# Performance work log

Hardware: AMD Instinct MI355X
Metric: run time of the kernel (lower is better)

Reference implementation:

```python
import jax, jax.numpy as jnp
import numpy as np

N_EMBD = 1024
N_HEAD = 16

def _lin_params(key, fan_in, fan_out):
    kw, kb = jax.random.split(key)
    bound = 1.0 / np.sqrt(fan_in)
    W = jax.random.uniform(kw, (fan_in, fan_out), minval=-bound, maxval=bound, dtype=jnp.float32)
    b = jax.random.uniform(kb, (fan_out,), minval=-bound, maxval=bound, dtype=jnp.float32)
    return W, b

def setup_inputs() -> dict:
    key = jax.random.key(0)
    ks = jax.random.split(key, 6)
    x = jax.random.normal(ks[0], (2, 2048, N_EMBD), dtype=jnp.float32)
    W_attn, b_attn = _lin_params(ks[1], N_EMBD, 3 * N_EMBD)
    W_proj, b_proj = _lin_params(ks[2], N_EMBD, N_EMBD)
    W_fc, b_fc = _lin_params(ks[3], N_EMBD, 4 * N_EMBD)
    W_fc2, b_fc2 = _lin_params(ks[4], 4 * N_EMBD, N_EMBD)
    ln1_g = jnp.ones((N_EMBD,), jnp.float32); ln1_b = jnp.zeros((N_EMBD,), jnp.float32)
    ln2_g = jnp.ones((N_EMBD,), jnp.float32); ln2_b = jnp.zeros((N_EMBD,), jnp.float32)
    return {"x": x, "W_attn": W_attn, "b_attn": b_attn, "W_proj": W_proj, "b_proj": b_proj,
            "W_fc": W_fc, "b_fc": b_fc, "W_fc2": W_fc2, "b_fc2": b_fc2,
            "ln1_g": ln1_g, "ln1_b": ln1_b, "ln2_g": ln2_g, "ln2_b": ln2_b}

def _layernorm(x, g, b, eps=1e-5):
    mu = jnp.mean(x, axis=-1, keepdims=True)
    var = jnp.var(x, axis=-1, keepdims=True)
    return (x - mu) * jax.lax.rsqrt(var + eps) * g + b

def _attention(x, W_attn, b_attn, W_proj, b_proj):
    B, T, C = x.shape
    hd = C // N_HEAD
    qkv = x @ W_attn + b_attn                      # [B,T,3C]
    q, k, v = jnp.split(qkv, 3, axis=-1)
    # [B,T,C] -> [B,H,T,hd]
    q = q.reshape(B, T, N_HEAD, hd).transpose(0, 2, 1, 3)
    k = k.reshape(B, T, N_HEAD, hd).transpose(0, 2, 1, 3)
    v = v.reshape(B, T, N_HEAD, hd).transpose(0, 2, 1, 3)
    att = jnp.einsum('bhqd,bhkd->bhqk', q, k) * (1.0 / np.sqrt(hd))
    causal = jnp.tril(jnp.ones((T, T), bool))
    att = jnp.where(causal[None, None], att, -jnp.inf)
    att = jax.nn.softmax(att, axis=-1)
    y = jnp.einsum('bhqk,bhkd->bhqd', att, v)      # [B,H,T,hd]
    y = y.transpose(0, 2, 1, 3).reshape(B, T, C)
    return y @ W_proj + b_proj

def _mlp(x, W_fc, b_fc, W_fc2, b_fc2):
    h = jax.nn.gelu(x @ W_fc + b_fc, approximate=False)
    return h @ W_fc2 + b_fc2

def reference(x, W_attn, b_attn, W_proj, b_proj, W_fc, b_fc, W_fc2, b_fc2,
              ln1_g, ln1_b, ln2_g, ln2_b):
    x = x + _attention(_layernorm(x, ln1_g, ln1_b), W_attn, b_attn, W_proj, b_proj)
    x = x + _mlp(_layernorm(x, ln2_g, ln2_b), W_fc, b_fc, W_fc2, b_fc2)
    return x
```

## Files before the change

### kernel.cpp

```cpp
#include <hip/hip_runtime.h>
#include <cstdint>
#include <cstddef>


typedef unsigned short u16;
typedef short bf16x8 __attribute__((ext_vector_type(8)));
typedef float f32x4 __attribute__((ext_vector_type(4)));

#define C_EMBD 1024
#define T_SEQ  2048
#define N_BATCH 2
#define N_HEADS 16
#define HEAD_D 64
#define M_TOK  4096
#define Q_SCALE 0.18033688011112042f

__device__ __forceinline__ u16 f2b(float f) {
  union { float f; unsigned u; } v; v.f = f;
  unsigned r = (v.u + 0x7fffu + ((v.u >> 16) & 1u)) >> 16;
  return (u16)r;
}
__device__ __forceinline__ float b2f(u16 u) {
  union { unsigned u; float f; } v; v.u = ((unsigned)u) << 16;
  return v.f;
}
__device__ __forceinline__ unsigned pk2(float a, float b) {
  union { float f; unsigned u; } x, y; x.f = a; y.f = b;
  return __builtin_amdgcn_perm(y.u, x.u, 0x07060302u);
}
__device__ __forceinline__ void load_lds16(const void* g, void* l) {
  __builtin_amdgcn_global_load_lds(
      (const __attribute__((address_space(1))) void*)g,
      (__attribute__((address_space(3))) void*)l, 16, 0, 0);
}
__device__ __forceinline__ float gelu_fast(float x) {
  const float p = x * __builtin_fmaf(0.044715f * x, x, 1.0f);
  const float t = __builtin_amdgcn_exp2f(2.3021859215f * p);
  return x * t * __builtin_amdgcn_rcpf(t + 1.0f);
}

__global__ __launch_bounds__(256) void transpose_cast(
    const float* __restrict__ W, u16* __restrict__ Wt, int K, int N) {
  __shared__ float tile[32][33];
  const int n0 = blockIdx.x * 32, k0 = blockIdx.y * 32;
  const int tx = threadIdx.x & 31, ty = threadIdx.x >> 5;
#pragma unroll
  for (int i = 0; i < 32; i += 8)
    tile[ty + i][tx] = W[(size_t)(k0 + ty + i) * N + n0 + tx];
  __syncthreads();
#pragma unroll
  for (int i = 0; i < 32; i += 8)
    Wt[(size_t)(n0 + ty + i) * K + k0 + tx] = f2b(tile[tx][ty + i]);
}

__global__ __launch_bounds__(256) void ln_cast(
    const float* __restrict__ X, const float* __restrict__ g,
    const float* __restrict__ b, u16* __restrict__ Y) {
  const int row = blockIdx.x;
  const int tid = threadIdx.x;
  const float4 v = ((const float4*)(X + (size_t)row * C_EMBD))[tid];
  float s = v.x + v.y + v.z + v.w;
  float ss = v.x * v.x + v.y * v.y + v.z * v.z + v.w * v.w;
#pragma unroll
  for (int off = 32; off > 0; off >>= 1) {
    s += __shfl_down(s, off, 64);
    ss += __shfl_down(ss, off, 64);
  }
  __shared__ float red[8];
  __shared__ float stats[2];
  const int wave = tid >> 6, lane = tid & 63;
  if (lane == 0) { red[wave] = s; red[4 + wave] = ss; }
  __syncthreads();
  if (tid == 0) {
    float S = red[0] + red[1] + red[2] + red[3];
    float SS = red[4] + red[5] + red[6] + red[7];
    float mu = S * (1.0f / C_EMBD);
    float var = SS * (1.0f / C_EMBD) - mu * mu;
    stats[0] = mu;
    stats[1] = rsqrtf(var + 1e-5f);
  }
  __syncthreads();
  const float mu = stats[0], rs = stats[1];
  const float4 gv = ((const float4*)g)[tid];
  const float4 bv = ((const float4*)b)[tid];
  ushort4 o;
  o.x = f2b((v.x - mu) * rs * gv.x + bv.x);
  o.y = f2b((v.y - mu) * rs * gv.y + bv.y);
  o.z = f2b((v.z - mu) * rs * gv.z + bv.z);
  o.w = f2b((v.w - mu) * rs * gv.w + bv.w);
  ((ushort4*)(Y + (size_t)row * C_EMBD))[tid] = o;
}

enum { EPI_BF16 = 0, EPI_GELU_BF16 = 2, EPI_PART = 3, EPI_QKV = 4 };

template <int EPI, int SPLIT>
__global__ __launch_bounds__(256) void gemm_bt(
    const u16* __restrict__ A, const u16* __restrict__ Bt,
    const float* __restrict__ bias,
    void* __restrict__ Cout, void* __restrict__ Cout2, void* __restrict__ Cout3,
    int M, int N, int K) {
  __shared__ u16 As[128 * 64];
  __shared__ u16 Bs[128 * 64];
  const int tid = threadIdx.x;
  const int wave = tid >> 6, lane = tid & 63;
  const int quad = lane >> 4, l16 = lane & 15;
  const int sw = l16 & 7;
  const int m0 = blockIdx.y * 128, n0 = blockIdx.x * 128;
  const int wm = (wave >> 1) * 64, wn = (wave & 1) * 64;

  f32x4 acc[4][4] = {};

  const int kTiles = (K >> 6) / SPLIT;
  const int kt0 = (SPLIT == 2) ? (int)blockIdx.z * kTiles : 0;
  for (int kt = kt0; kt < kt0 + kTiles; ++kt) {
    const int k0 = kt << 6;
#pragma unroll
    for (int i = 0; i < 4; ++i) {
      const int c = tid + i * 256;
      const int row = c >> 3, gc = ((c & 7) ^ (row & 7)) * 8;
      load_lds16(A + (size_t)(m0 + row) * K + k0 + gc, &As[c * 8]);
    }
#pragma unroll
    for (int i = 0; i < 4; ++i) {
      const int c = tid + i * 256;
      const int row = c >> 3, gc = ((c & 7) ^ (row & 7)) * 8;
      load_lds16(Bt + (size_t)(n0 + row) * K + k0 + gc, &Bs[c * 8]);
    }
    __syncthreads();
#pragma unroll
    for (int ks = 0; ks < 2; ++ks) {
      bf16x8 aF[4], bF[4];
#pragma unroll
      for (int t = 0; t < 4; ++t) {
        aF[t] = *(const bf16x8*)
            &As[(wm + t * 16 + l16) * 64 + (((ks * 4 + quad) ^ sw) * 8)];
        bF[t] = *(const bf16x8*)
            &Bs[(wn + t * 16 + l16) * 64 + (((ks * 4 + quad) ^ sw) * 8)];
      }
#pragma unroll
      for (int tm = 0; tm < 4; ++tm)
#pragma unroll
        for (int tn = 0; tn < 4; ++tn)
          acc[tm][tn] = __builtin_amdgcn_mfma_f32_16x16x32_bf16(
              bF[tn], aF[tm], acc[tm][tn], 0, 0, 0);
    }
    __syncthreads();
  }

  float* Pz = (float*)((SPLIT == 2 && blockIdx.z == 1) ? Cout2 : Cout);
#pragma unroll
  for (int tm = 0; tm < 4; ++tm) {
    const int row = m0 + wm + tm * 16 + l16;
#pragma unroll
    for (int tn = 0; tn < 4; ++tn) {
      const int col = n0 + wn + tn * 16 + quad * 4;
      if constexpr (EPI == EPI_PART) {
        *(float4*)&Pz[(size_t)row * N + col] = *(float4*)&acc[tm][tn];
      } else if constexpr (EPI == EPI_QKV) {
        const int bb = row >> 11, t = row & (T_SEQ - 1);
        const float4 bz = *(const float4*)&bias[col];
        float v0 = acc[tm][tn][0] + bz.x, v1 = acc[tm][tn][1] + bz.y;
        float v2 = acc[tm][tn][2] + bz.z, v3 = acc[tm][tn][3] + bz.w;
        const int sec = col >> 10;
        const int h = (col & 1023) >> 6, d4 = col & 63;
        const int bh = bb * N_HEADS + h;
        if (sec == 0) {
          ushort4 o;
          o.x = f2b(v0 * Q_SCALE); o.y = f2b(v1 * Q_SCALE);
          o.z = f2b(v2 * Q_SCALE); o.w = f2b(v3 * Q_SCALE);
          *(ushort4*)&((u16*)Cout)[((size_t)bh * T_SEQ + t) * HEAD_D + d4] = o;
        } else if (sec == 1) {
          ushort4 o;
          o.x = f2b(v0); o.y = f2b(v1); o.z = f2b(v2); o.w = f2b(v3);
          *(ushort4*)&((u16*)Cout2)[((size_t)bh * T_SEQ + t) * HEAD_D + d4] = o;
        } else {
          u16* vp = (u16*)Cout3 + ((size_t)bh * HEAD_D + d4) * T_SEQ + t;
          vp[0] = f2b(v0); vp[T_SEQ] = f2b(v1);
          vp[2 * T_SEQ] = f2b(v2); vp[3 * T_SEQ] = f2b(v3);
        }
      } else {
        const float4 bz = *(const float4*)&bias[col];
        float v0 = acc[tm][tn][0] + bz.x, v1 = acc[tm][tn][1] + bz.y;
        float v2 = acc[tm][tn][2] + bz.z, v3 = acc[tm][tn][3] + bz.w;
        if constexpr (EPI == EPI_GELU_BF16) {
          v0 = gelu_fast(v0); v1 = gelu_fast(v1);
          v2 = gelu_fast(v2); v3 = gelu_fast(v3);
        }
        ushort4 o;
        o.x = f2b(v0); o.y = f2b(v1); o.z = f2b(v2); o.w = f2b(v3);
        *(ushort4*)&((u16*)Cout)[(size_t)row * N + col] = o;
      }
    }
  }
}

__global__ __launch_bounds__(256) void reduce_add(
    const float* __restrict__ P0, const float* __restrict__ P1,
    const float* __restrict__ bias, const float* __restrict__ res,
    float* __restrict__ out) {
  const int idx = blockIdx.x * 256 + threadIdx.x;
  const float4 a = ((const float4*)P0)[idx];
  const float4 b = ((const float4*)P1)[idx];
  const float4 c = ((const float4*)res)[idx];
  const float4 g = ((const float4*)bias)[idx & 255];
  float4 o;
  o.x = a.x + b.x + c.x + g.x;
  o.y = a.y + b.y + c.y + g.y;
  o.z = a.z + b.z + c.z + g.z;
  o.w = a.w + b.w + c.w + g.w;
  ((float4*)out)[idx] = o;
}

__global__ __launch_bounds__(256) void attn_fwd(
    const u16* __restrict__ Q, const u16* __restrict__ Kb,
    const u16* __restrict__ Vt, u16* __restrict__ Y) {
  const int bh = blockIdx.y;
  const int pair = blockIdx.x;
  const int nqt = (int)(T_SEQ / 64);
  const int tid = threadIdx.x;
  const int wave = tid >> 6, lane = tid & 63;
  const int quad = lane >> 4, l16 = lane & 15;
  const int sw = l16 & 7;
  const u16* Qp = Q + (size_t)bh * T_SEQ * HEAD_D;
  const u16* Kp = Kb + (size_t)bh * T_SEQ * HEAD_D;
  const u16* Vp = Vt + (size_t)bh * HEAD_D * T_SEQ;

  __shared__ u16 Ks[2][64 * 64];
  __shared__ u16 Vs[2][64 * 64];
  __shared__ u16 Pl[4][16 * 72];

  const int c1 = tid, c2 = tid + 256;
  const int r1 = c1 >> 3, g1 = ((c1 & 7) ^ (r1 & 7)) * 8;
  const int r2 = c2 >> 3, g2 = ((c2 & 7) ^ (r2 & 7)) * 8;
  const size_t kO1 = (size_t)r1 * HEAD_D + g1, kO2 = (size_t)r2 * HEAD_D + g2;
  const size_t vO1 = (size_t)r1 * T_SEQ + g1, vO2 = (size_t)r2 * T_SEQ + g2;
  u16* const dK1[2] = {&Ks[0][c1 * 8], &Ks[1][c1 * 8]};
  u16* const dK2[2] = {&Ks[0][c2 * 8], &Ks[1][c2 * 8]};
  u16* const dV1[2] = {&Vs[0][c1 * 8], &Vs[1][c1 * 8]};
  u16* const dV2[2] = {&Vs[0][c2 * 8], &Vs[1][c2 * 8]};

  auto stageK = [&](int bb, int k0) {
    const u16* base = Kp + (size_t)k0 * HEAD_D;
    load_lds16(base + kO1, dK1[bb]);
    load_lds16(base + kO2, dK2[bb]);
  };
  auto stageV = [&](int bb, int k0) {
    const u16* base = Vp + k0;
    load_lds16(base + vO1, dV1[bb]);
    load_lds16(base + vO2, dV2[bb]);
  };

  const int b = bh >> 4, h = bh & 15;

#pragma unroll 1
  for (int phase = 0; phase < 2; ++phase) {
    const int qb = phase == 0 ? (nqt - 1 - pair) : pair;
    const int q0 = qb * 64;
    const int qglob = q0 + wave * 16 + l16;

    if (phase == 1) __syncthreads();

    bf16x8 qF[2];
    qF[0] = *(const bf16x8*)&Qp[(size_t)qglob * HEAD_D + quad * 8];
    qF[1] = *(const bf16x8*)&Qp[(size_t)qglob * HEAD_D + 32 + quad * 8];

    f32x4 o[4] = {};
    float mrun = -3e38f, lrun = 0.0f;

    stageK(0, 0);
    stageV(0, 0);

    int buf = 0;
    for (int kb = 0; kb <= qb; ++kb) {
      const int k0 = kb * 64;
      __syncthreads();
      if (kb < qb) {
        stageK(buf ^ 1, k0 + 64);
        stageV(buf ^ 1, k0 + 64);
      }
      f32x4 st[4] = {};
#pragma unroll
      for (int ks = 0; ks < 2; ++ks) {
#pragma unroll
        for (int nt = 0; nt < 4; ++nt) {
          bf16x8 kF = *(const bf16x8*)
              &Ks[buf][(nt * 16 + l16) * 64 + (((ks * 4 + quad) ^ sw) * 8)];
          st[nt] = __builtin_amdgcn_mfma_f32_16x16x32_bf16(kF, qF[ks], st[nt],
                                                           0, 0, 0);
        }
      }
      if (kb == qb) {
#pragma unroll
        for (int nt = 0; nt < 4; ++nt) {
#pragma unroll
          for (int r = 0; r < 4; ++r) {
            const int key = k0 + nt * 16 + quad * 4 + r;
            if (key > qglob) st[nt][r] = -3e38f;
          }
        }
      }
      float m = st[0][0];
#pragma unroll
      for (int nt = 0; nt < 4; ++nt)
#pragma unroll
        for (int r = 0; r < 4; ++r) m = fmaxf(m, st[nt][r]);
      m = fmaxf(m, __shfl_xor(m, 16, 64));
      m = fmaxf(m, __shfl_xor(m, 32, 64));
      const float nm = fmaxf(mrun, m);
      const float alpha = __builtin_amdgcn_exp2f(mrun - nm);
      mrun = nm;
      float sum = 0.0f;
#pragma unroll
      for (int nt = 0; nt < 4; ++nt)
#pragma unroll
        for (int r = 0; r < 4; ++r) {
          const float p = __builtin_amdgcn_exp2f(st[nt][r] - nm);
          st[nt][r] = p;
          sum += p;
        }
      sum += __shfl_xor(sum, 16, 64);
      sum += __shfl_xor(sum, 32, 64);
      lrun = lrun * alpha + sum;
#pragma unroll
      for (int nt = 0; nt < 4; ++nt)
#pragma unroll
        for (int r = 0; r < 4; ++r) o[nt][r] *= alpha;
#pragma unroll
      for (int nt = 0; nt < 4; ++nt) {
        uint2 pk;
        pk.x = pk2(st[nt][0], st[nt][1]);
        pk.y = pk2(st[nt][2], st[nt][3]);
        *(uint2*)&Pl[wave][l16 * 72 + nt * 16 + quad * 4] = pk;
      }
#pragma unroll
      for (int ks = 0; ks < 2; ++ks) {
        bf16x8 aP = *(const bf16x8*)&Pl[wave][l16 * 72 + ks * 32 + quad * 8];
#pragma unroll
        for (int nt = 0; nt < 4; ++nt) {
          bf16x8 vF = *(const bf16x8*)
              &Vs[buf][(nt * 16 + l16) * 64 + (((ks * 4 + quad) ^ sw) * 8)];
          o[nt] =
              __builtin_amdgcn_mfma_f32_16x16x32_bf16(vF, aP, o[nt], 0, 0, 0);
        }
      }
      buf ^= 1;
    }

    const float rl = 1.0f / lrun;
    u16* yp = Y + ((size_t)(b * T_SEQ + qglob)) * C_EMBD + h * HEAD_D;
#pragma unroll
    for (int nt = 0; nt < 4; ++nt) {
      ushort4 ov;
      ov.x = f2b(o[nt][0] * rl); ov.y = f2b(o[nt][1] * rl);
      ov.z = f2b(o[nt][2] * rl); ov.w = f2b(o[nt][3] * rl);
      *(ushort4*)&yp[nt * 16 + quad * 4] = ov;
    }
  }
}

extern "C" void kernel_launch(void* const* d_in, const int* in_sizes, int n_in,
                              void* d_out, int out_size, void* d_ws,
                              size_t ws_size, hipStream_t stream) {
  const float* x      = (const float*)d_in[0];
  const float* W_attn = (const float*)d_in[1];
  const float* b_attn = (const float*)d_in[2];
  const float* W_proj = (const float*)d_in[3];
  const float* b_proj = (const float*)d_in[4];
  const float* W_fc   = (const float*)d_in[5];
  const float* b_fc   = (const float*)d_in[6];
  const float* W_fc2  = (const float*)d_in[7];
  const float* b_fc2  = (const float*)d_in[8];
  const float* ln1_g  = (const float*)d_in[9];
  const float* ln1_b  = (const float*)d_in[10];
  const float* ln2_g  = (const float*)d_in[11];
  const float* ln2_b  = (const float*)d_in[12];

  u16* wqkvT = (u16*)d_ws;
  u16* wprojT = wqkvT + (size_t)3072 * 1024;
  u16* wfcT  = wprojT + (size_t)1024 * 1024;
  u16* wfc2T = wfcT + (size_t)4096 * 1024;
  u16* Abuf  = wfc2T + (size_t)1024 * 4096;
  float* x1  = (float*)(Abuf + (size_t)M_TOK * C_EMBD);
  u16* hbuf  = (u16*)(x1 + (size_t)M_TOK * C_EMBD);
  float* projP = (float*)hbuf;
  u16* Qb    = hbuf + (size_t)M_TOK * 4096;
  u16* Kbuf  = Qb + (size_t)32 * T_SEQ * HEAD_D;
  u16* Vtb   = Kbuf + (size_t)32 * T_SEQ * HEAD_D;
  float* fc2P1 = (float*)Qb;

  const dim3 blk(256);

  transpose_cast<<<dim3(3072 / 32, 1024 / 32), blk, 0, stream>>>(W_attn, wqkvT, 1024, 3072);
  transpose_cast<<<dim3(1024 / 32, 1024 / 32), blk, 0, stream>>>(W_proj, wprojT, 1024, 1024);
  transpose_cast<<<dim3(4096 / 32, 1024 / 32), blk, 0, stream>>>(W_fc, wfcT, 1024, 4096);
  transpose_cast<<<dim3(1024 / 32, 4096 / 32), blk, 0, stream>>>(W_fc2, wfc2T, 4096, 1024);

  ln_cast<<<M_TOK, blk, 0, stream>>>(x, ln1_g, ln1_b, Abuf);

  gemm_bt<EPI_QKV, 1><<<dim3(3072 / 128, M_TOK / 128), blk, 0, stream>>>(
      Abuf, wqkvT, b_attn, Qb, Kbuf, Vtb, M_TOK, 3072, 1024);

  attn_fwd<<<dim3(T_SEQ / 128, 32), blk, 0, stream>>>(Qb, Kbuf, Vtb, Abuf);

  gemm_bt<EPI_PART, 2><<<dim3(1024 / 128, M_TOK / 128, 2), blk, 0, stream>>>(
      Abuf, wprojT, nullptr, projP, projP + (size_t)M_TOK * C_EMBD, nullptr,
      M_TOK, 1024, 1024);
  reduce_add<<<M_TOK * C_EMBD / 1024, blk, 0, stream>>>(
      projP, projP + (size_t)M_TOK * C_EMBD, b_proj, x, x1);

  ln_cast<<<M_TOK, blk, 0, stream>>>(x1, ln2_g, ln2_b, Abuf);

  gemm_bt<EPI_GELU_BF16, 1><<<dim3(4096 / 128, M_TOK / 128), blk, 0, stream>>>(
      Abuf, wfcT, b_fc, hbuf, nullptr, nullptr, M_TOK, 4096, 1024);

  gemm_bt<EPI_PART, 2><<<dim3(1024 / 128, M_TOK / 128, 2), blk, 0, stream>>>(
      hbuf, wfc2T, nullptr, d_out, fc2P1, nullptr, M_TOK, 1024, 4096);
  reduce_add<<<M_TOK * C_EMBD / 1024, blk, 0, stream>>>(
      (const float*)d_out, fc2P1, b_fc2, x1, (float*)d_out);
}
```

Baseline: 362.2 us.

## Fuse residual epilogue, drop split-K, merge transposes, remap block IDs

```diff
diff --git a/kernel.cpp b/kernel.cpp
--- a/kernel.cpp
+++ b/kernel.cpp
@@ -39,10 +39,20 @@
   return x * t * __builtin_amdgcn_rcpf(t + 1.0f);
 }
 
-__global__ __launch_bounds__(256) void transpose_cast(
-    const float* __restrict__ W, u16* __restrict__ Wt, int K, int N) {
+__global__ __launch_bounds__(256) void transpose_cast_all(
+    const float* __restrict__ W0, u16* __restrict__ D0,
+    const float* __restrict__ W1, u16* __restrict__ D1,
+    const float* __restrict__ W2, u16* __restrict__ D2,
+    const float* __restrict__ W3, u16* __restrict__ D3) {
+  int id = blockIdx.x;
+  const float* W; u16* D; int K, N, t;
+  if (id < 3072)      { W = W0; D = D0; K = 1024; N = 3072; t = id; }
+  else if (id < 4096) { W = W1; D = D1; K = 1024; N = 1024; t = id - 3072; }
+  else if (id < 8192) { W = W2; D = D2; K = 1024; N = 4096; t = id - 4096; }
+  else                { W = W3; D = D3; K = 4096; N = 1024; t = id - 8192; }
+  const int nTN = N >> 5;
+  const int n0 = (t % nTN) * 32, k0 = (t / nTN) * 32;
   __shared__ float tile[32][33];
-  const int n0 = blockIdx.x * 32, k0 = blockIdx.y * 32;
   const int tx = threadIdx.x & 31, ty = threadIdx.x >> 5;
 #pragma unroll
   for (int i = 0; i < 32; i += 8)
@@ -50,7 +60,7 @@
   __syncthreads();
 #pragma unroll
   for (int i = 0; i < 32; i += 8)
-    Wt[(size_t)(n0 + ty + i) * K + k0 + tx] = f2b(tile[tx][ty + i]);
+    D[(size_t)(n0 + ty + i) * K + k0 + tx] = f2b(tile[tx][ty + i]);
 }
 
 __global__ __launch_bounds__(256) void ln_cast(
@@ -91,71 +101,94 @@
   ((ushort4*)(Y + (size_t)row * C_EMBD))[tid] = o;
 }
 
-enum { EPI_BF16 = 0, EPI_GELU_BF16 = 2, EPI_PART = 3, EPI_QKV = 4 };
-
-template <int EPI, int SPLIT>
+enum { EPI_BF16 = 0, EPI_RES_F32 = 1, EPI_GELU_BF16 = 2, EPI_QKV = 4 };
+
+template <int EPI, int BN>
 __global__ __launch_bounds__(256) void gemm_bt(
     const u16* __restrict__ A, const u16* __restrict__ Bt,
-    const float* __restrict__ bias,
+    const float* __restrict__ bias, const float* __restrict__ res,
     void* __restrict__ Cout, void* __restrict__ Cout2, void* __restrict__ Cout3,
     int M, int N, int K) {
+  constexpr int TB = BN / 32;
   __shared__ u16 As[128 * 64];
-  __shared__ u16 Bs[128 * 64];
+  __shared__ u16 Bs[BN * 64];
   const int tid = threadIdx.x;
   const int wave = tid >> 6, lane = tid & 63;
   const int quad = lane >> 4, l16 = lane & 15;
   const int sw = l16 & 7;
-  const int m0 = blockIdx.y * 128, n0 = blockIdx.x * 128;
-  const int wm = (wave >> 1) * 64, wn = (wave & 1) * 64;
-
-  f32x4 acc[4][4] = {};
-
-  const int kTiles = (K >> 6) / SPLIT;
-  const int kt0 = (SPLIT == 2) ? (int)blockIdx.z * kTiles : 0;
-  for (int kt = kt0; kt < kt0 + kTiles; ++kt) {
+
+  const int id = (int)blockIdx.y * (int)gridDim.x + (int)blockIdx.x;
+  const int mt = ((id & 7) << 2) + ((id >> 3) & 3);
+  const int nt_ = id >> 5;
+  const int m0 = mt * 128, n0 = nt_ * BN;
+
+  const int wm = (wave >> 1) * 64, wn = (wave & 1) * (BN / 2);
+
+  f32x4 acc[4][TB] = {};
+
+  size_t aOff[4], bOff[TB];
+  int aLds[4], bLds[TB];
+#pragma unroll
+  for (int i = 0; i < 4; ++i) {
+    const int c = tid + i * 256;
+    const int row = c >> 3, gc = ((c & 7) ^ (row & 7)) * 8;
+    aOff[i] = (size_t)(m0 + row) * K + gc;
+    aLds[i] = c * 8;
+  }
+#pragma unroll
+  for (int i = 0; i < TB; ++i) {
+    const int c = tid + i * 256;
+    const int row = c >> 3, gc = ((c & 7) ^ (row & 7)) * 8;
+    bOff[i] = (size_t)(n0 + row) * K + gc;
+    bLds[i] = c * 8;
+  }
+
+  const int kTiles = K >> 6;
+  for (int kt = 0; kt < kTiles; ++kt) {
     const int k0 = kt << 6;
 #pragma unroll
-    for (int i = 0; i < 4; ++i) {
-      const int c = tid + i * 256;
-      const int row = c >> 3, gc = ((c & 7) ^ (row & 7)) * 8;
-      load_lds16(A + (size_t)(m0 + row) * K + k0 + gc, &As[c * 8]);
-    }
-#pragma unroll
-    for (int i = 0; i < 4; ++i) {
-      const int c = tid + i * 256;
-      const int row = c >> 3, gc = ((c & 7) ^ (row & 7)) * 8;
-      load_lds16(Bt + (size_t)(n0 + row) * K + k0 + gc, &Bs[c * 8]);
-    }
+    for (int i = 0; i < 4; ++i)
+      load_lds16(A + aOff[i] + k0, &As[aLds[i]]);
+#pragma unroll
+    for (int i = 0; i < TB; ++i)
+      load_lds16(Bt + bOff[i] + k0, &Bs[bLds[i]]);
     __syncthreads();
 #pragma unroll
     for (int ks = 0; ks < 2; ++ks) {
-      bf16x8 aF[4], bF[4];
-#pragma unroll
-      for (int t = 0; t < 4; ++t) {
+      bf16x8 aF[4], bF[TB];
+#pragma unroll
+      for (int t = 0; t < 4; ++t)
         aF[t] = *(const bf16x8*)
             &As[(wm + t * 16 + l16) * 64 + (((ks * 4 + quad) ^ sw) * 8)];
+#pragma unroll
+      for (int t = 0; t < TB; ++t)
         bF[t] = *(const bf16x8*)
             &Bs[(wn + t * 16 + l16) * 64 + (((ks * 4 + quad) ^ sw) * 8)];
-      }
 #pragma unroll
       for (int tm = 0; tm < 4; ++tm)
 #pragma unroll
-        for (int tn = 0; tn < 4; ++tn)
+        for (int tn = 0; tn < TB; ++tn)
           acc[tm][tn] = __builtin_amdgcn_mfma_f32_16x16x32_bf16(
               bF[tn], aF[tm], acc[tm][tn], 0, 0, 0);
     }
     __syncthreads();
   }
 
-  float* Pz = (float*)((SPLIT == 2 && blockIdx.z == 1) ? Cout2 : Cout);
 #pragma unroll
   for (int tm = 0; tm < 4; ++tm) {
     const int row = m0 + wm + tm * 16 + l16;
 #pragma unroll
-    for (int tn = 0; tn < 4; ++tn) {
+    for (int tn = 0; tn < TB; ++tn) {
       const int col = n0 + wn + tn * 16 + quad * 4;
-      if constexpr (EPI == EPI_PART) {
-        *(float4*)&Pz[(size_t)row * N + col] = *(float4*)&acc[tm][tn];
+      if constexpr (EPI == EPI_RES_F32) {
+        const float4 bz = *(const float4*)&bias[col];
+        const float4 rz = *(const float4*)&res[(size_t)row * N + col];
+        float4 o;
+        o.x = acc[tm][tn][0] + bz.x + rz.x;
+        o.y = acc[tm][tn][1] + bz.y + rz.y;
+        o.z = acc[tm][tn][2] + bz.z + rz.z;
+        o.w = acc[tm][tn][3] + bz.w + rz.w;
+        *(float4*)&((float*)Cout)[(size_t)row * N + col] = o;
       } else if constexpr (EPI == EPI_QKV) {
         const int bb = row >> 11, t = row & (T_SEQ - 1);
         const float4 bz = *(const float4*)&bias[col];
@@ -194,28 +227,12 @@
   }
 }
 
-__global__ __launch_bounds__(256) void reduce_add(
-    const float* __restrict__ P0, const float* __restrict__ P1,
-    const float* __restrict__ bias, const float* __restrict__ res,
-    float* __restrict__ out) {
-  const int idx = blockIdx.x * 256 + threadIdx.x;
-  const float4 a = ((const float4*)P0)[idx];
-  const float4 b = ((const float4*)P1)[idx];
-  const float4 c = ((const float4*)res)[idx];
-  const float4 g = ((const float4*)bias)[idx & 255];
-  float4 o;
-  o.x = a.x + b.x + c.x + g.x;
-  o.y = a.y + b.y + c.y + g.y;
-  o.z = a.z + b.z + c.z + g.z;
-  o.w = a.w + b.w + c.w + g.w;
-  ((float4*)out)[idx] = o;
-}
-
 __global__ __launch_bounds__(256) void attn_fwd(
     const u16* __restrict__ Q, const u16* __restrict__ Kb,
     const u16* __restrict__ Vt, u16* __restrict__ Y) {
-  const int bh = blockIdx.y;
-  const int pair = blockIdx.x;
+  const int id = (int)blockIdx.y * (int)gridDim.x + (int)blockIdx.x;
+  const int bh = (id & 7) + (((id >> 3) & 3) << 3);
+  const int pair = id >> 5;
   const int nqt = (int)(T_SEQ / 64);
   const int tid = threadIdx.x;
   const int wave = tid >> 6, lane = tid & 63;
@@ -382,39 +399,30 @@
   u16* Abuf  = wfc2T + (size_t)1024 * 4096;
   float* x1  = (float*)(Abuf + (size_t)M_TOK * C_EMBD);
   u16* hbuf  = (u16*)(x1 + (size_t)M_TOK * C_EMBD);
-  float* projP = (float*)hbuf;
   u16* Qb    = hbuf + (size_t)M_TOK * 4096;
   u16* Kbuf  = Qb + (size_t)32 * T_SEQ * HEAD_D;
   u16* Vtb   = Kbuf + (size_t)32 * T_SEQ * HEAD_D;
-  float* fc2P1 = (float*)Qb;
 
   const dim3 blk(256);
 
-  transpose_cast<<<dim3(3072 / 32, 1024 / 32), blk, 0, stream>>>(W_attn, wqkvT, 1024, 3072);
-  transpose_cast<<<dim3(1024 / 32, 1024 / 32), blk, 0, stream>>>(W_proj, wprojT, 1024, 1024);
-  transpose_cast<<<dim3(4096 / 32, 1024 / 32), blk, 0, stream>>>(W_fc, wfcT, 1024, 4096);
-  transpose_cast<<<dim3(1024 / 32, 4096 / 32), blk, 0, stream>>>(W_fc2, wfc2T, 4096, 1024);
+  transpose_cast_all<<<12288, blk, 0, stream>>>(
+      W_attn, wqkvT, W_proj, wprojT, W_fc, wfcT, W_fc2, wfc2T);
 
   ln_cast<<<M_TOK, blk, 0, stream>>>(x, ln1_g, ln1_b, Abuf);
 
-  gemm_bt<EPI_QKV, 1><<<dim3(3072 / 128, M_TOK / 128), blk, 0, stream>>>(
-      Abuf, wqkvT, b_attn, Qb, Kbuf, Vtb, M_TOK, 3072, 1024);
+  gemm_bt<EPI_QKV, 128><<<dim3(3072 / 128, M_TOK / 128), blk, 0, stream>>>(
+      Abuf, wqkvT, b_attn, nullptr, Qb, Kbuf, Vtb, M_TOK, 3072, 1024);
 
   attn_fwd<<<dim3(T_SEQ / 128, 32), blk, 0, stream>>>(Qb, Kbuf, Vtb, Abuf);
 
-  gemm_bt<EPI_PART, 2><<<dim3(1024 / 128, M_TOK / 128, 2), blk, 0, stream>>>(
-      Abuf, wprojT, nullptr, projP, projP + (size_t)M_TOK * C_EMBD, nullptr,
-      M_TOK, 1024, 1024);
-  reduce_add<<<M_TOK * C_EMBD / 1024, blk, 0, stream>>>(
-      projP, projP + (size_t)M_TOK * C_EMBD, b_proj, x, x1);
+  gemm_bt<EPI_RES_F32, 64><<<dim3(1024 / 64, M_TOK / 128), blk, 0, stream>>>(
+      Abuf, wprojT, b_proj, x, x1, nullptr, nullptr, M_TOK, 1024, 1024);
 
   ln_cast<<<M_TOK, blk, 0, stream>>>(x1, ln2_g, ln2_b, Abuf);
 
-  gemm_bt<EPI_GELU_BF16, 1><<<dim3(4096 / 128, M_TOK / 128), blk, 0, stream>>>(
-      Abuf, wfcT, b_fc, hbuf, nullptr, nullptr, M_TOK, 4096, 1024);
-
-  gemm_bt<EPI_PART, 2><<<dim3(1024 / 128, M_TOK / 128, 2), blk, 0, stream>>>(
-      hbuf, wfc2T, nullptr, d_out, fc2P1, nullptr, M_TOK, 1024, 4096);
-  reduce_add<<<M_TOK * C_EMBD / 1024, blk, 0, stream>>>(
-      (const float*)d_out, fc2P1, b_fc2, x1, (float*)d_out);
-}
+  gemm_bt<EPI_GELU_BF16, 128><<<dim3(4096 / 128, M_TOK / 128), blk, 0, stream>>>(
+      Abuf, wfcT, b_fc, nullptr, hbuf, nullptr, nullptr, M_TOK, 4096, 1024);
+
+  gemm_bt<EPI_RES_F32, 64><<<dim3(1024 / 64, M_TOK / 128), blk, 0, stream>>>(
+      hbuf, wfc2T, b_fc2, x1, d_out, nullptr, nullptr, M_TOK, 1024, 4096);
+}
```

Measured after the change: 334.6 us. 7.6% less time.
